# Kernel optimization log

Hardware: AMD Instinct MI355X
Metric: run time of the kernel (lower is better)

Reference implementation:

```python
import jax, jax.numpy as jnp
import numpy as np

N_EMBD = 2048
N_Q = 32
N_KV = 8
GROUP = N_Q // N_KV   # 4
HD = N_EMBD // N_Q    # 64
BASE = 10000.0
NEG_INF = -1e30


def _rope(x):
    """Rotate-half RoPE on last dim; positions 1..t along dim -2 (as in the
    original _build_cache which uses arange(1, seq_len+1))."""
    t, d = x.shape[-2], x.shape[-1]
    d2 = d // 2
    theta = 1.0 / (BASE ** (jnp.arange(0, d, 2, dtype=jnp.float32) / d))  # (d/2,)
    pos = jnp.arange(1, t + 1, dtype=jnp.float32)                          # (t,)
    ang = pos[:, None] * theta[None, :]                                    # (t, d/2)
    ang = jnp.concatenate([ang, ang], axis=-1)                             # (t, d)
    sin, cos = jnp.sin(ang), jnp.cos(ang)
    rot = jnp.concatenate([-x[..., d2:], x[..., :d2]], axis=-1)
    return x * cos + rot * sin


def setup_inputs() -> dict:
    key = jax.random.key(0)
    ks = jax.random.split(key, 5)
    b, t = 2, 1024
    s = 1.0 / np.sqrt(N_EMBD)
    return {
        "x": jax.random.normal(ks[0], (b, t, N_EMBD), dtype=jnp.float32),
        "wq": jax.random.normal(ks[1], (N_EMBD, N_EMBD), dtype=jnp.float32) * s,
        "bq": jnp.zeros((N_EMBD,), dtype=jnp.float32),
        "wk": jax.random.normal(ks[2], (N_EMBD, N_KV * HD), dtype=jnp.float32) * s,
        "bk": jnp.zeros((N_KV * HD,), dtype=jnp.float32),
        "wv": jax.random.normal(ks[3], (N_EMBD, N_KV * HD), dtype=jnp.float32) * s,
        "bv": jnp.zeros((N_KV * HD,), dtype=jnp.float32),
        "wo": jax.random.normal(ks[4], (N_EMBD, N_EMBD), dtype=jnp.float32) * s,
        "bo": jnp.zeros((N_EMBD,), dtype=jnp.float32),
    }


def reference(x, wq, bq, wk, bk, wv, bv, wo, bo):
    b, t, _ = x.shape
    q = x @ wq + bq                                   # (b, t, E)
    k = x @ wk + bk                                   # (b, t, NKV*HD)
    v = x @ wv + bv
    q = q.reshape(b, t, N_Q, HD).transpose(0, 2, 1, 3)        # (b, nq, t, d)
    q = q.reshape(b, N_KV, GROUP, t, HD)                      # (b, hkv, g, t, d)
    k = k.reshape(b, t, N_KV, HD).transpose(0, 2, 1, 3)       # (b, hkv, t, d)
    v = v.reshape(b, t, N_KV, HD).transpose(0, 2, 1, 3)
    q = _rope(q)
    k = _rope(k)
    scale = jnp.sqrt(jnp.float32(HD))
    att = jnp.einsum("bhgqd,bhkd->bhgqk", q, k) / scale       # (b, hkv, g, t, t)
    causal = jnp.tril(jnp.ones((t, t), dtype=bool))
    att = jnp.where(causal, att, NEG_INF)
    att = jax.nn.softmax(att, axis=-1)
    out = jnp.einsum("bhgqk,bhkd->bhgqd", att, v)             # (b, hkv, g, t, d)
    out = out.transpose(0, 3, 1, 2, 4).reshape(b, t, N_EMBD)  # (b, t, E)
    return out @ wo + bo
```

## Files before the change

### kernel.cpp

```cpp
#include <hip/hip_runtime.h>
#include <hip/hip_bf16.h>
#include <cstdint>


typedef __attribute__((ext_vector_type(8))) short short8;
typedef __attribute__((ext_vector_type(4))) short short4v;
typedef __attribute__((ext_vector_type(4))) float f32x4;

__device__ inline short f2b(float f) {
  union { float f; unsigned u; } v; v.f = f;
  unsigned r = v.u + 0x7fffu + ((v.u >> 16) & 1u);
  return (short)(r >> 16);
}

__device__ inline float exp2_fast(float x) {
  float r;
  asm("v_exp_f32 %0, %1" : "=v"(r) : "v"(x));
  return r;
}

__device__ inline void gl_lds16(const void* g, void* l) {
  __builtin_amdgcn_global_load_lds((const __attribute__((address_space(1))) void*)g,
                                   (__attribute__((address_space(3))) void*)l,
                                   16, 0, 0);
}

__global__ void cast_x_kernel(const float* __restrict__ x, short* __restrict__ xb, int n4) {
  int i = blockIdx.x * 256 + threadIdx.x;
  if (i >= n4) return;
  float4 v = ((const float4*)x)[i];
  short4v o; o.x = f2b(v.x); o.y = f2b(v.y); o.z = f2b(v.z); o.w = f2b(v.w);
  ((short4v*)xb)[i] = o;
}

__global__ void wtrans_all(const float* __restrict__ wq, const float* __restrict__ wk,
                           const float* __restrict__ wv, const float* __restrict__ wo,
                           short* __restrict__ WqkvT, short* __restrict__ woT) {
  __shared__ float tile[64][65];
  const int bx = blockIdx.x;
  const float* W; short* WT; int N, off, nb;
  if (bx < 32)      { W = wq; WT = WqkvT; N = 2048; off = 0;    nb = bx * 64; }
  else if (bx < 40) { W = wk; WT = WqkvT; N = 512;  off = 2048; nb = (bx - 32) * 64; }
  else if (bx < 48) { W = wv; WT = WqkvT; N = 512;  off = 2560; nb = (bx - 40) * 64; }
  else              { W = wo; WT = woT;   N = 2048; off = 0;    nb = (bx - 48) * 64; }
  const int kb = blockIdx.y * 64;
  const int tid = threadIdx.x;
  const int c = tid & 63, r0 = tid >> 6;
#pragma unroll
  for (int s = 0; s < 16; ++s) {
    int k = r0 + s * 4;
    tile[c][k] = W[(size_t)(kb + k) * N + nb + c];
  }
  __syncthreads();
#pragma unroll
  for (int s = 0; s < 16; ++s) {
    int n = r0 + s * 4;
    WT[(size_t)(off + nb + n) * 2048 + kb + c] = f2b(tile[n][c]);
  }
}

__device__ __forceinline__ void gemm_loop_bk64(const short* __restrict__ Ag,
                                               const short* __restrict__ Bg,
                                               short* lA, short* lB,
                                               int w, int l15, int q4,
                                               f32x4 acc[2][4]) {
  const int K = 2048, NS = 32;
  const int q4x = q4 ^ ((l15 >> 1) & 3);
  auto stage = [&](int s, int d) {
    const short* As = Ag + s * 64;
    const short* Bs = Bg + s * 64;
    short* a = lA + d * 8192 + w * 512;
    gl_lds16(As, a);
    gl_lds16(As + 64 * K, a + 2048);
    gl_lds16(As + 32, a + 4096);
    gl_lds16(As + 64 * K + 32, a + 6144);
    short* bp = lB + d * 4096 + w * 512;
    gl_lds16(Bs, bp);
    gl_lds16(Bs + 32, bp + 2048);
  };
  stage(0, 0);
  for (int s = 0; s < NS; ++s) {
    const int d = s & 1;
    __syncthreads();
    if (s + 1 < NS) stage(s + 1, d ^ 1);
#pragma unroll
    for (int ks = 0; ks < 2; ++ks) {
      const short* ap = lA + d * 8192 + ks * 4096;
      const short* bp = lB + d * 4096 + ks * 2048;
      short8 af[2], bf[4];
#pragma unroll
      for (int mf = 0; mf < 2; ++mf) af[mf] = *(const short8*)(ap + (w * 32 + mf * 16 + l15) * 32 + q4x * 8);
#pragma unroll
      for (int nf = 0; nf < 4; ++nf) bf[nf] = *(const short8*)(bp + (nf * 16 + l15) * 32 + q4x * 8);
#pragma unroll
      for (int mf = 0; mf < 2; ++mf)
#pragma unroll
        for (int nf = 0; nf < 4; ++nf)
          acc[mf][nf] = __builtin_amdgcn_mfma_f32_16x16x32_bf16(af[mf], bf[nf], acc[mf][nf], 0, 0, 0);
    }
  }
}

__launch_bounds__(256, 3)
__global__ void gemm_qkv(const short* __restrict__ A, const short* __restrict__ BT,
                         const float* __restrict__ bq, const float* __restrict__ bk,
                         const float* __restrict__ bv,
                         short* __restrict__ Qb, short* __restrict__ Kb,
                         short* __restrict__ VTb) {
  __shared__ __align__(16) short lA[16384];
  __shared__ __align__(16) short lB[8192];
  const int K = 2048;
  const int tid = threadIdx.x, lane = tid & 63, w = tid >> 6;
  const int q4 = lane >> 4, l15 = lane & 15;
  const int bn = blockIdx.x * 64, bm = blockIdx.y * 128;

  const int swzc = ((tid & 3) ^ ((tid >> 3) & 3)) << 3;
  const short* Ag = A + (size_t)(bm + (tid >> 2)) * K + swzc;
  const short* Bg = BT + (size_t)(bn + (tid >> 2)) * K + swzc;

  f32x4 acc[2][4];
  const f32x4 fz = {0.f, 0.f, 0.f, 0.f};
#pragma unroll
  for (int i = 0; i < 2; ++i)
#pragma unroll
    for (int j = 0; j < 4; ++j) acc[i][j] = fz;

  gemm_loop_bk64(Ag, Bg, lA, lB, w, l15, q4, acc);

  const float L2T = 0.4152410118609203f;
  const float theta_a = exp2_fast(-(float)l15 * L2T);
  const float theta_b = exp2_fast(-(float)(l15 + 16) * L2T);
  const float s2 = 0.18033688011112042f;

  if (bn < 2048) {
    const int h = bn >> 6;
    float bb0 = bq[bn + l15], bb1 = bq[bn + 16 + l15], bb2 = bq[bn + 32 + l15], bb3 = bq[bn + 48 + l15];
#pragma unroll
    for (int mf = 0; mf < 2; ++mf)
#pragma unroll
      for (int r = 0; r < 4; ++r) {
        int row = bm + w * 32 + mf * 16 + q4 * 4 + r;
        int batch = row >> 10, t = row & 1023;
        float pos = (float)(t + 1);
        float sa, ca, sb, cb;
        __sincosf(pos * theta_a, &sa, &ca);
        __sincosf(pos * theta_b, &sb, &cb);
        float x0 = acc[mf][0][r] + bb0, x2 = acc[mf][2][r] + bb2;
        float x1 = acc[mf][1][r] + bb1, x3 = acc[mf][3][r] + bb3;
        size_t base = ((size_t)(batch * 32 + h) * 1024 + t) * 64;
        Qb[base + l15]      = f2b((x0 * ca - x2 * sa) * s2);
        Qb[base + l15 + 32] = f2b((x2 * ca + x0 * sa) * s2);
        Qb[base + l15 + 16] = f2b((x1 * cb - x3 * sb) * s2);
        Qb[base + l15 + 48] = f2b((x3 * cb + x1 * sb) * s2);
      }
  } else if (bn < 2560) {
    const int co = bn - 2048;
    const int hkv = co >> 6;
    float bb0 = bk[co + l15], bb1 = bk[co + 16 + l15], bb2 = bk[co + 32 + l15], bb3 = bk[co + 48 + l15];
#pragma unroll
    for (int mf = 0; mf < 2; ++mf)
#pragma unroll
      for (int r = 0; r < 4; ++r) {
        int row = bm + w * 32 + mf * 16 + q4 * 4 + r;
        int batch = row >> 10, t = row & 1023;
        float pos = (float)(t + 1);
        float sa, ca, sb, cb;
        __sincosf(pos * theta_a, &sa, &ca);
        __sincosf(pos * theta_b, &sb, &cb);
        float x0 = acc[mf][0][r] + bb0, x2 = acc[mf][2][r] + bb2;
        float x1 = acc[mf][1][r] + bb1, x3 = acc[mf][3][r] + bb3;
        size_t base = (size_t)(batch * 8 + hkv) * 65536 + t * 32;
        Kb[base + l15]              = f2b(x0 * ca - x2 * sa);
        Kb[base + l15 + 16]         = f2b(x1 * cb - x3 * sb);
        Kb[base + 32768 + l15]      = f2b(x2 * ca + x0 * sa);
        Kb[base + 32768 + l15 + 16] = f2b(x3 * cb + x1 * sb);
      }
  } else {
    const int co = bn - 2560;
    const int hkv = co >> 6;
    float bb[4];
#pragma unroll
    for (int nf = 0; nf < 4; ++nf) bb[nf] = bv[co + nf * 16 + l15];
    const int batch = (bm + w * 32) >> 10;
    const size_t vbase = (size_t)(batch * 8 + hkv) * 65536;
#pragma unroll
    for (int mf = 0; mf < 2; ++mf) {
      const int t0 = (bm + w * 32 + mf * 16 + q4 * 4) & 1023;
      const size_t rbase = vbase + (size_t)(t0 >> 5) * 2048 + (t0 & 31);
#pragma unroll
      for (int nf = 0; nf < 4; ++nf) {
        short4v pk;
#pragma unroll
        for (int r = 0; r < 4; ++r) pk[r] = f2b(acc[mf][nf][r] + bb[nf]);
        *(short4v*)(VTb + rbase + (nf * 16 + l15) * 32) = pk;
      }
    }
  }
}

#define PROW 72
__launch_bounds__(256, 3)
__global__ void attn8_kernel(const short* __restrict__ Qb, const short* __restrict__ Kb,
                             const short* __restrict__ VTb, short* __restrict__ AO) {
  __shared__ __align__(16) short lK[2][2 * 64 * 32];
  __shared__ __align__(16) short lVT[2][2 * 64 * 32];
  __shared__ __align__(16) short lP[4][2][16 * PROW];
  const int tid = threadIdx.x, lane = tid & 63, w = tid >> 6;
  const int q4 = lane >> 4, l15 = lane & 15;
  const int q4x = q4 ^ ((l15 >> 1) & 3);
  const int swzc = ((tid & 3) ^ ((tid >> 3) & 3)) << 3;
  const int qt = (int)gridDim.x - 1 - (int)blockIdx.x;
  const int h = blockIdx.y, b = blockIdx.z;
  const int hkv = h >> 2;
  const int qb = qt * 128 + w * 32;
  const int kdiag = qb >> 6;
  const int ns = 2 * qt + 2;

  const short* Qg = Qb + (size_t)(b * 32 + h) * 65536;
  const short* Kg = Kb + (size_t)(b * 8 + hkv) * 65536;
  const short* Vg = VTb + (size_t)(b * 8 + hkv) * 65536;

  short8 qf[2][2];
#pragma unroll
  for (int mf = 0; mf < 2; ++mf) {
    const short* qr = Qg + (size_t)(qb + mf * 16 + l15) * 64 + q4 * 8;
    qf[mf][0] = *(const short8*)(qr);
    qf[mf][1] = *(const short8*)(qr + 32);
  }

  const f32x4 fz = {0.f, 0.f, 0.f, 0.f};
  f32x4 o[2][4], ol[2];
#pragma unroll
  for (int mf = 0; mf < 2; ++mf) {
    ol[mf] = fz;
#pragma unroll
    for (int i = 0; i < 4; ++i) o[mf][i] = fz;
  }
  short8 ones;
#pragma unroll
  for (int i = 0; i < 8; ++i) ones[i] = (short)0x3F80;

  auto stage = [&](int s, int d) {
    const short* Ksrc = Kg + (size_t)(s * 64 + (tid >> 2)) * 32 + swzc;
    short* kd = (short*)lK + d * 4096 + w * 512;
    gl_lds16(Ksrc, kd);
    gl_lds16(Ksrc + 32768, kd + 2048);
    const short* Vsrc = Vg + (size_t)(2 * s) * 2048 + (tid >> 2) * 32 + swzc;
    short* vd = (short*)lVT + d * 4096 + w * 512;
    gl_lds16(Vsrc, vd);
    gl_lds16(Vsrc + 2048, vd + 2048);
  };

  stage(0, 0);
  for (int s = 0; s < ns; ++s) {
    const int d = s & 1;
    __syncthreads();
    if (s + 1 < ns) stage(s + 1, d ^ 1);
    if (s <= kdiag) {
      const short* kp = (short*)lK + d * 4096;
      const short* vp = (short*)lVT + d * 4096;
      short8 kf0[4], kf1[4];
#pragma unroll
      for (int nt = 0; nt < 4; ++nt) {
        kf0[nt] = *(const short8*)(kp + (nt * 16 + l15) * 32 + q4x * 8);
        kf1[nt] = *(const short8*)(kp + 2048 + (nt * 16 + l15) * 32 + q4x * 8);
      }
      f32x4 sv[2][4];
#pragma unroll
      for (int mf = 0; mf < 2; ++mf)
#pragma unroll
        for (int nt = 0; nt < 4; ++nt) {
          f32x4 z = __builtin_amdgcn_mfma_f32_16x16x32_bf16(qf[mf][0], kf0[nt], fz, 0, 0, 0);
          sv[mf][nt] = __builtin_amdgcn_mfma_f32_16x16x32_bf16(qf[mf][1], kf1[nt], z, 0, 0, 0);
        }
      if (s == kdiag) {
#pragma unroll
        for (int mf = 0; mf < 2; ++mf)
#pragma unroll
          for (int r = 0; r < 4; ++r) {
            const int qrow = qb + mf * 16 + q4 * 4 + r;
            const int col = s * 64 + l15;
#pragma unroll
            for (int nt = 0; nt < 4; ++nt)
              if (col + nt * 16 > qrow) sv[mf][nt][r] = -1e30f;
          }
      }
#pragma unroll
      for (int mf = 0; mf < 2; ++mf) {
        short* lPm = lP[w][mf];
#pragma unroll
        for (int r = 0; r < 4; ++r)
#pragma unroll
          for (int nt = 0; nt < 4; ++nt)
            lPm[(q4 * 4 + r) * PROW + nt * 16 + l15] = f2b(exp2_fast(sv[mf][nt][r] - 16.f));
      }
      short8 vf0[4], vf1[4];
#pragma unroll
      for (int dt = 0; dt < 4; ++dt) {
        vf0[dt] = *(const short8*)(vp + (dt * 16 + l15) * 32 + q4x * 8);
        vf1[dt] = *(const short8*)(vp + 2048 + (dt * 16 + l15) * 32 + q4x * 8);
      }
#pragma unroll
      for (int mf = 0; mf < 2; ++mf) {
        const short* lPm = lP[w][mf];
        short8 pf0 = *(const short8*)(lPm + l15 * PROW + q4 * 8);
        short8 pf1 = *(const short8*)(lPm + l15 * PROW + 32 + q4 * 8);
        ol[mf] = __builtin_amdgcn_mfma_f32_16x16x32_bf16(pf0, ones, ol[mf], 0, 0, 0);
        ol[mf] = __builtin_amdgcn_mfma_f32_16x16x32_bf16(pf1, ones, ol[mf], 0, 0, 0);
#pragma unroll
        for (int dt = 0; dt < 4; ++dt) {
          o[mf][dt] = __builtin_amdgcn_mfma_f32_16x16x32_bf16(pf0, vf0[dt], o[mf][dt], 0, 0, 0);
          o[mf][dt] = __builtin_amdgcn_mfma_f32_16x16x32_bf16(pf1, vf1[dt], o[mf][dt], 0, 0, 0);
        }
      }
    }
  }

#pragma unroll
  for (int mf = 0; mf < 2; ++mf)
#pragma unroll
    for (int r = 0; r < 4; ++r) {
      float inv = __builtin_amdgcn_rcpf(ol[mf][r]);
      int row = qb + mf * 16 + q4 * 4 + r;
#pragma unroll
      for (int dt = 0; dt < 4; ++dt)
        AO[(size_t)(b * 1024 + row) * 2048 + h * 64 + dt * 16 + l15] = f2b(o[mf][dt][r] * inv);
    }
}

__launch_bounds__(256, 3)
__global__ void gemm_out(const short* __restrict__ A, const short* __restrict__ BT,
                         float* __restrict__ C, const float* __restrict__ bias,
                         int N, int K) {
  __shared__ __align__(16) short lA[16384];
  __shared__ __align__(16) short lB[8192];
  const int tid = threadIdx.x, lane = tid & 63, w = tid >> 6;
  const int q4 = lane >> 4, l15 = lane & 15;
  const int bn = blockIdx.x * 64, bm = blockIdx.y * 128;

  const int swzc = ((tid & 3) ^ ((tid >> 3) & 3)) << 3;
  const short* Ag = A + (size_t)(bm + (tid >> 2)) * K + swzc;
  const short* Bg = BT + (size_t)(bn + (tid >> 2)) * K + swzc;

  f32x4 acc[2][4];
  const f32x4 fz = {0.f, 0.f, 0.f, 0.f};
#pragma unroll
  for (int i = 0; i < 2; ++i)
#pragma unroll
    for (int j = 0; j < 4; ++j) acc[i][j] = fz;

  gemm_loop_bk64(Ag, Bg, lA, lB, w, l15, q4, acc);

#pragma unroll
  for (int mf = 0; mf < 2; ++mf)
#pragma unroll
    for (int nf = 0; nf < 4; ++nf) {
      int col = bn + nf * 16 + l15;
      float bb = bias[col];
#pragma unroll
      for (int r = 0; r < 4; ++r) {
        int row = bm + w * 32 + mf * 16 + q4 * 4 + r;
        C[(size_t)row * N + col] = acc[mf][nf][r] + bb;
      }
    }
}

extern "C" void kernel_launch(void* const* d_in, const int* in_sizes, int n_in,
                              void* d_out, int out_size, void* d_ws, size_t ws_size,
                              hipStream_t stream) {
  const float* x  = (const float*)d_in[0];
  const float* wq = (const float*)d_in[1];
  const float* bq = (const float*)d_in[2];
  const float* wk = (const float*)d_in[3];
  const float* bk = (const float*)d_in[4];
  const float* wv = (const float*)d_in[5];
  const float* bv = (const float*)d_in[6];
  const float* wo = (const float*)d_in[7];
  const float* bo = (const float*)d_in[8];
  float* out = (float*)d_out;
  const int B = in_sizes[0] / (1024 * 2048);
  const int M = B * 1024;

  char* ws = (char*)d_ws;
  size_t off = 0;
  auto alloc = [&](size_t bytes) -> char* {
    char* p = ws + off;
    off += (bytes + 255) & ~(size_t)255;
    return p;
  };
  short* xb    = (short*)alloc((size_t)M * 2048 * 2);
  short* WqkvT = (short*)alloc((size_t)3072 * 2048 * 2);
  short* woT   = (short*)alloc((size_t)2048 * 2048 * 2);
  short* Qb    = (short*)alloc((size_t)B * 32 * 1024 * 64 * 2);
  short* Kb    = (short*)alloc((size_t)B * 8 * 2 * 1024 * 32 * 2);
  short* VTb   = (short*)alloc((size_t)B * 8 * 32 * 64 * 32 * 2);
  short* AO    = (short*)alloc((size_t)M * 2048 * 2);

  cast_x_kernel<<<(M * 2048 / 4 + 255) / 256, 256, 0, stream>>>(x, xb, M * 2048 / 4);
  wtrans_all<<<dim3(80, 32), 256, 0, stream>>>(wq, wk, wv, wo, WqkvT, woT);
  gemm_qkv<<<dim3(48, M / 128), 256, 0, stream>>>(xb, WqkvT, bq, bk, bv, Qb, Kb, VTb);
  attn8_kernel<<<dim3(8, 32, B), 256, 0, stream>>>(Qb, Kb, VTb, AO);
  gemm_out<<<dim3(32, M / 128), 256, 0, stream>>>(AO, woT, out, bo, 2048, 2048);
}
```

Measured before the change: 206.6 us.

## Pair complementary causal query tiles per attention block and fuse prep kernels

The attention kernel now gives each block two 64-row query tiles (j and 15-j), processed one after the other over a fixed 17-step K/V pipeline, so every block does the same amount of causal work. Before, blocks owned 128-row tiles whose work grew with position. Each warp now holds 16 query rows instead of 32, which halves per-warp MFMA density and reloads the K/V tiles for the second query tile. Separately, the x cast and the weight transposes are merged into one launch to save a kernel launch.

```diff
diff --git a/kernel.cpp b/kernel.cpp
--- a/kernel.cpp
+++ b/kernel.cpp
@@ -25,26 +25,28 @@
                                    16, 0, 0);
 }
 
-__global__ void cast_x_kernel(const float* __restrict__ x, short* __restrict__ xb, int n4) {
-  int i = blockIdx.x * 256 + threadIdx.x;
-  if (i >= n4) return;
-  float4 v = ((const float4*)x)[i];
-  short4v o; o.x = f2b(v.x); o.y = f2b(v.y); o.z = f2b(v.z); o.w = f2b(v.w);
-  ((short4v*)xb)[i] = o;
-}
-
-__global__ void wtrans_all(const float* __restrict__ wq, const float* __restrict__ wk,
-                           const float* __restrict__ wv, const float* __restrict__ wo,
-                           short* __restrict__ WqkvT, short* __restrict__ woT) {
+__global__ void prep_all(const float* __restrict__ x, const float* __restrict__ wq,
+                         const float* __restrict__ wk, const float* __restrict__ wv,
+                         const float* __restrict__ wo, short* __restrict__ xb,
+                         short* __restrict__ WqkvT, short* __restrict__ woT, int n4) {
   __shared__ float tile[64][65];
   const int bx = blockIdx.x;
+  const int tid = threadIdx.x;
+  if (bx >= 80) {
+    int i = ((bx - 80) * 32 + blockIdx.y) * 256 + tid;
+    if (i < n4) {
+      float4 v = ((const float4*)x)[i];
+      short4v o; o.x = f2b(v.x); o.y = f2b(v.y); o.z = f2b(v.z); o.w = f2b(v.w);
+      ((short4v*)xb)[i] = o;
+    }
+    return;
+  }
   const float* W; short* WT; int N, off, nb;
   if (bx < 32)      { W = wq; WT = WqkvT; N = 2048; off = 0;    nb = bx * 64; }
   else if (bx < 40) { W = wk; WT = WqkvT; N = 512;  off = 2048; nb = (bx - 32) * 64; }
   else if (bx < 48) { W = wv; WT = WqkvT; N = 512;  off = 2560; nb = (bx - 40) * 64; }
   else              { W = wo; WT = woT;   N = 2048; off = 0;    nb = (bx - 48) * 64; }
   const int kb = blockIdx.y * 64;
-  const int tid = threadIdx.x;
   const int c = tid & 63, r0 = tid >> 6;
 #pragma unroll
   for (int s = 0; s < 16; ++s) {
@@ -200,132 +202,131 @@
 
 #define PROW 72
 __launch_bounds__(256, 3)
-__global__ void attn8_kernel(const short* __restrict__ Qb, const short* __restrict__ Kb,
+__global__ void attn9_kernel(const short* __restrict__ Qb, const short* __restrict__ Kb,
                              const short* __restrict__ VTb, short* __restrict__ AO) {
-  __shared__ __align__(16) short lK[2][2 * 64 * 32];
-  __shared__ __align__(16) short lVT[2][2 * 64 * 32];
-  __shared__ __align__(16) short lP[4][2][16 * PROW];
+  __shared__ __align__(16) short lK[2 * 4096];
+  __shared__ __align__(16) short lVT[2 * 4096];
+  __shared__ __align__(16) short lP[4][16 * PROW];
   const int tid = threadIdx.x, lane = tid & 63, w = tid >> 6;
   const int q4 = lane >> 4, l15 = lane & 15;
   const int q4x = q4 ^ ((l15 >> 1) & 3);
   const int swzc = ((tid & 3) ^ ((tid >> 3) & 3)) << 3;
-  const int qt = (int)gridDim.x - 1 - (int)blockIdx.x;
+  const int pr = blockIdx.x;
+  const int jA = pr, jB = 15 - pr;
   const int h = blockIdx.y, b = blockIdx.z;
   const int hkv = h >> 2;
-  const int qb = qt * 128 + w * 32;
-  const int kdiag = qb >> 6;
-  const int ns = 2 * qt + 2;
 
   const short* Qg = Qb + (size_t)(b * 32 + h) * 65536;
   const short* Kg = Kb + (size_t)(b * 8 + hkv) * 65536;
   const short* Vg = VTb + (size_t)(b * 8 + hkv) * 65536;
 
-  short8 qf[2][2];
-#pragma unroll
-  for (int mf = 0; mf < 2; ++mf) {
-    const short* qr = Qg + (size_t)(qb + mf * 16 + l15) * 64 + q4 * 8;
-    qf[mf][0] = *(const short8*)(qr);
-    qf[mf][1] = *(const short8*)(qr + 32);
+  short8 qfA0, qfA1, qfB0, qfB1;
+  {
+    const short* qr = Qg + (size_t)(jA * 64 + w * 16 + l15) * 64 + q4 * 8;
+    qfA0 = *(const short8*)(qr); qfA1 = *(const short8*)(qr + 32);
+    const short* qr2 = Qg + (size_t)(jB * 64 + w * 16 + l15) * 64 + q4 * 8;
+    qfB0 = *(const short8*)(qr2); qfB1 = *(const short8*)(qr2 + 32);
   }
 
   const f32x4 fz = {0.f, 0.f, 0.f, 0.f};
-  f32x4 o[2][4], ol[2];
-#pragma unroll
-  for (int mf = 0; mf < 2; ++mf) {
-    ol[mf] = fz;
-#pragma unroll
-    for (int i = 0; i < 4; ++i) o[mf][i] = fz;
-  }
+  f32x4 o[4], ol;
   short8 ones;
 #pragma unroll
   for (int i = 0; i < 8; ++i) ones[i] = (short)0x3F80;
 
-  auto stage = [&](int s, int d) {
-    const short* Ksrc = Kg + (size_t)(s * 64 + (tid >> 2)) * 32 + swzc;
-    short* kd = (short*)lK + d * 4096 + w * 512;
+  auto stage = [&](int kt, int d) {
+    const short* Ksrc = Kg + (size_t)(kt * 64 + (tid >> 2)) * 32 + swzc;
+    short* kd = lK + d * 4096 + w * 512;
     gl_lds16(Ksrc, kd);
     gl_lds16(Ksrc + 32768, kd + 2048);
-    const short* Vsrc = Vg + (size_t)(2 * s) * 2048 + (tid >> 2) * 32 + swzc;
-    short* vd = (short*)lVT + d * 4096 + w * 512;
+    const short* Vsrc = Vg + (size_t)(2 * kt) * 2048 + (tid >> 2) * 32 + swzc;
+    short* vd = lVT + d * 4096 + w * 512;
     gl_lds16(Vsrc, vd);
     gl_lds16(Vsrc + 2048, vd + 2048);
   };
 
+  auto comp = [&](int d, int kt, int jt, short8 qf0, short8 qf1) {
+    const short* kp = lK + d * 4096;
+    const short* vp = lVT + d * 4096;
+    short8 kf0[4], kf1[4];
+#pragma unroll
+    for (int nt = 0; nt < 4; ++nt) {
+      kf0[nt] = *(const short8*)(kp + (nt * 16 + l15) * 32 + q4x * 8);
+      kf1[nt] = *(const short8*)(kp + 2048 + (nt * 16 + l15) * 32 + q4x * 8);
+    }
+    f32x4 sv[4];
+#pragma unroll
+    for (int nt = 0; nt < 4; ++nt) {
+      f32x4 z = __builtin_amdgcn_mfma_f32_16x16x32_bf16(qf0, kf0[nt], fz, 0, 0, 0);
+      sv[nt] = __builtin_amdgcn_mfma_f32_16x16x32_bf16(qf1, kf1[nt], z, 0, 0, 0);
+    }
+    if (kt == jt) {
+#pragma unroll
+      for (int r = 0; r < 4; ++r) {
+        const int qrow = jt * 64 + w * 16 + q4 * 4 + r;
+        const int col = kt * 64 + l15;
+#pragma unroll
+        for (int nt = 0; nt < 4; ++nt)
+          if (col + nt * 16 > qrow) sv[nt][r] = -1e30f;
+      }
+    }
+    short* lPm = lP[w];
+#pragma unroll
+    for (int r = 0; r < 4; ++r)
+#pragma unroll
+      for (int nt = 0; nt < 4; ++nt)
+        lPm[(q4 * 4 + r) * PROW + nt * 16 + l15] = f2b(exp2_fast(sv[nt][r] - 16.f));
+    short8 vf0[4], vf1[4];
+#pragma unroll
+    for (int dt = 0; dt < 4; ++dt) {
+      vf0[dt] = *(const short8*)(vp + (dt * 16 + l15) * 32 + q4x * 8);
+      vf1[dt] = *(const short8*)(vp + 2048 + (dt * 16 + l15) * 32 + q4x * 8);
+    }
+    short8 pf0 = *(const short8*)(lPm + l15 * PROW + q4 * 8);
+    short8 pf1 = *(const short8*)(lPm + l15 * PROW + 32 + q4 * 8);
+    ol = __builtin_amdgcn_mfma_f32_16x16x32_bf16(pf0, ones, ol, 0, 0, 0);
+    ol = __builtin_amdgcn_mfma_f32_16x16x32_bf16(pf1, ones, ol, 0, 0, 0);
+#pragma unroll
+    for (int dt = 0; dt < 4; ++dt) {
+      o[dt] = __builtin_amdgcn_mfma_f32_16x16x32_bf16(pf0, vf0[dt], o[dt], 0, 0, 0);
+      o[dt] = __builtin_amdgcn_mfma_f32_16x16x32_bf16(pf1, vf1[dt], o[dt], 0, 0, 0);
+    }
+  };
+
+  auto emit = [&](int jt) {
+#pragma unroll
+    for (int r = 0; r < 4; ++r) {
+      float inv = __builtin_amdgcn_rcpf(ol[r]);
+      int row = jt * 64 + w * 16 + q4 * 4 + r;
+#pragma unroll
+      for (int dt = 0; dt < 4; ++dt)
+        AO[(size_t)(b * 1024 + row) * 2048 + h * 64 + dt * 16 + l15] = f2b(o[dt][r] * inv);
+    }
+  };
+
+  ol = fz;
+#pragma unroll
+  for (int dt = 0; dt < 4; ++dt) o[dt] = fz;
+
+  const int nsA = jA + 1;
   stage(0, 0);
-  for (int s = 0; s < ns; ++s) {
+  for (int s = 0; s < 17; ++s) {
     const int d = s & 1;
     __syncthreads();
-    if (s + 1 < ns) stage(s + 1, d ^ 1);
-    if (s <= kdiag) {
-      const short* kp = (short*)lK + d * 4096;
-      const short* vp = (short*)lVT + d * 4096;
-      short8 kf0[4], kf1[4];
-#pragma unroll
-      for (int nt = 0; nt < 4; ++nt) {
-        kf0[nt] = *(const short8*)(kp + (nt * 16 + l15) * 32 + q4x * 8);
-        kf1[nt] = *(const short8*)(kp + 2048 + (nt * 16 + l15) * 32 + q4x * 8);
-      }
-      f32x4 sv[2][4];
-#pragma unroll
-      for (int mf = 0; mf < 2; ++mf)
-#pragma unroll
-        for (int nt = 0; nt < 4; ++nt) {
-          f32x4 z = __builtin_amdgcn_mfma_f32_16x16x32_bf16(qf[mf][0], kf0[nt], fz, 0, 0, 0);
-          sv[mf][nt] = __builtin_amdgcn_mfma_f32_16x16x32_bf16(qf[mf][1], kf1[nt], z, 0, 0, 0);
-        }
-      if (s == kdiag) {
-#pragma unroll
-        for (int mf = 0; mf < 2; ++mf)
-#pragma unroll
-          for (int r = 0; r < 4; ++r) {
-            const int qrow = qb + mf * 16 + q4 * 4 + r;
-            const int col = s * 64 + l15;
-#pragma unroll
-            for (int nt = 0; nt < 4; ++nt)
-              if (col + nt * 16 > qrow) sv[mf][nt][r] = -1e30f;
-          }
-      }
-#pragma unroll
-      for (int mf = 0; mf < 2; ++mf) {
-        short* lPm = lP[w][mf];
-#pragma unroll
-        for (int r = 0; r < 4; ++r)
-#pragma unroll
-          for (int nt = 0; nt < 4; ++nt)
-            lPm[(q4 * 4 + r) * PROW + nt * 16 + l15] = f2b(exp2_fast(sv[mf][nt][r] - 16.f));
-      }
-      short8 vf0[4], vf1[4];
-#pragma unroll
-      for (int dt = 0; dt < 4; ++dt) {
-        vf0[dt] = *(const short8*)(vp + (dt * 16 + l15) * 32 + q4x * 8);
-        vf1[dt] = *(const short8*)(vp + 2048 + (dt * 16 + l15) * 32 + q4x * 8);
-      }
-#pragma unroll
-      for (int mf = 0; mf < 2; ++mf) {
-        const short* lPm = lP[w][mf];
-        short8 pf0 = *(const short8*)(lPm + l15 * PROW + q4 * 8);
-        short8 pf1 = *(const short8*)(lPm + l15 * PROW + 32 + q4 * 8);
-        ol[mf] = __builtin_amdgcn_mfma_f32_16x16x32_bf16(pf0, ones, ol[mf], 0, 0, 0);
-        ol[mf] = __builtin_amdgcn_mfma_f32_16x16x32_bf16(pf1, ones, ol[mf], 0, 0, 0);
-#pragma unroll
-        for (int dt = 0; dt < 4; ++dt) {
-          o[mf][dt] = __builtin_amdgcn_mfma_f32_16x16x32_bf16(pf0, vf0[dt], o[mf][dt], 0, 0, 0);
-          o[mf][dt] = __builtin_amdgcn_mfma_f32_16x16x32_bf16(pf1, vf1[dt], o[mf][dt], 0, 0, 0);
-        }
-      }
-    }
-  }
-
-#pragma unroll
-  for (int mf = 0; mf < 2; ++mf)
-#pragma unroll
-    for (int r = 0; r < 4; ++r) {
-      float inv = __builtin_amdgcn_rcpf(ol[mf][r]);
-      int row = qb + mf * 16 + q4 * 4 + r;
-#pragma unroll
-      for (int dt = 0; dt < 4; ++dt)
-        AO[(size_t)(b * 1024 + row) * 2048 + h * 64 + dt * 16 + l15] = f2b(o[mf][dt][r] * inv);
-    }
+    if (s + 1 < 17) stage((s + 1 < nsA) ? s + 1 : s + 1 - nsA, d ^ 1);
+    if (s < nsA) {
+      comp(d, s, jA, qfA0, qfA1);
+    } else {
+      if (s == nsA) {
+        emit(jA);
+        ol = fz;
+#pragma unroll
+        for (int dt = 0; dt < 4; ++dt) o[dt] = fz;
+      }
+      comp(d, s - nsA, jB, qfB0, qfB1);
+    }
+  }
+  emit(jB);
 }
 
 __launch_bounds__(256, 3)
@@ -396,9 +397,10 @@
   short* VTb   = (short*)alloc((size_t)B * 8 * 32 * 64 * 32 * 2);
   short* AO    = (short*)alloc((size_t)M * 2048 * 2);
 
-  cast_x_kernel<<<(M * 2048 / 4 + 255) / 256, 256, 0, stream>>>(x, xb, M * 2048 / 4);
-  wtrans_all<<<dim3(80, 32), 256, 0, stream>>>(wq, wk, wv, wo, WqkvT, woT);
+  const int n4 = M * 2048 / 4;
+  const int nbc = (n4 + 255) / 256;
+  prep_all<<<dim3(80 + (nbc + 31) / 32, 32), 256, 0, stream>>>(x, wq, wk, wv, wo, xb, WqkvT, woT, n4);
   gemm_qkv<<<dim3(48, M / 128), 256, 0, stream>>>(xb, WqkvT, bq, bk, bv, Qb, Kb, VTb);
-  attn8_kernel<<<dim3(8, 32, B), 256, 0, stream>>>(Qb, Kb, VTb, AO);
+  attn9_kernel<<<dim3(8, 32, B), 256, 0, stream>>>(Qb, Kb, VTb, AO);
   gemm_out<<<dim3(32, M / 128), 256, 0, stream>>>(AO, woT, out, bo, 2048, 2048);
 }
```

Result: faster. 196.6 us (-4.8%).
